# Optimization experiments

Hardware: AMD Instinct MI355X
Metric: run time of the kernel (lower is better)

## Reference

```python
import jax, jax.numpy as jnp
import numpy as np
import math

EPSILON = 1e-5
B, P, H, W = 64, 68, 64, 64


def setup_inputs() -> dict:
    key = jax.random.key(0)
    k1, k2, k3 = jax.random.split(key, 3)
    # probability heatmaps: positive, normalized over spatial dims
    hm = jax.random.uniform(k1, (B, P, H, W), dtype=jnp.float32) + 1e-3
    hm = hm / jnp.sum(hm, axis=(2, 3), keepdims=True)
    # means in pixel coordinates [0, W)
    means = jax.random.uniform(k2, (B, P, 2), dtype=jnp.float32) * (W - 1)
    # SPD 2x2 covariance, flattened to 4: Sigma = A A^T + c*I
    A = jax.random.normal(k3, (B, P, 2, 2), dtype=jnp.float32) * 2.0
    Sigma = jnp.einsum('bpij,bpkj->bpik', A, A) + 2.0 * jnp.eye(2, dtype=jnp.float32)
    covariance = Sigma.reshape(B, P, 4)
    return {"heatmaps": hm, "means": means, "covariance": covariance}


def reference(heatmaps, means, covariance):
    b, p, h, w = heatmaps.shape
    # grid: xv[i,j] = j, yv[i,j] = i
    yv, xv = jnp.meshgrid(jnp.arange(h, dtype=heatmaps.dtype),
                          jnp.arange(w, dtype=heatmaps.dtype), indexing='ij')
    Sigma = covariance.reshape(b, p, 2, 2)
    s00, s01 = Sigma[:, :, 0, 0], Sigma[:, :, 0, 1]
    s10, s11 = Sigma[:, :, 1, 0], Sigma[:, :, 1, 1]
    det = s00 * s11 - s01 * s10 + EPSILON                       # [b,p]
    # centered coordinates, [b,p,h,w]
    dx = xv[None, None] - means[:, :, 0, None, None]
    dy = yv[None, None] - means[:, :, 1, None, None]
    # quadratic form v^T Sigma^{-1} v with Sigma^{-1} = adj(Sigma)/det
    quad = (s11[..., None, None] * dx * dx
            - (s01 + s10)[..., None, None] * dx * dy
            + s00[..., None, None] * dy * dy) / det[..., None, None]
    log_prob_2 = -0.5 * quad
    prob = jnp.exp(log_prob_2) / (2.0 * math.pi * jnp.sqrt(det)[..., None, None])
    prob = prob / jnp.sum(prob, axis=(2, 3), keepdims=True)
    # KLDivLoss(reduce=False): target * (log target - input), target = heatmaps (detached)
    hm = heatmaps.reshape(b * p, h * w)
    pr = prob.reshape(b * p, h * w)
    kld = jax.scipy.special.xlogy(hm, hm) - hm * jnp.log(pr + EPSILON)
    loss = jnp.sum(kld, axis=1).mean()
    return loss
```

## Files before the change

kernel.cpp:

```cpp
#include <hip/hip_runtime.h>
#include <math.h>

#define EPS 1e-5f

constexpr int Bc = 64, Pc = 68, Hc = 64, Wc = 64;
constexpr int NPIX  = Hc * Wc;
constexpr int NTILE = Bc * Pc;
constexpr int BLK   = 256;
constexpr int PPT   = NPIX / BLK;

__device__ __forceinline__ float block_reduce_sum(float v, float* sbuf) {
    __syncthreads();
    #pragma unroll
    for (int o = 32; o > 0; o >>= 1) v += __shfl_down(v, o, 64);
    const int lane = threadIdx.x & 63;
    const int wid  = threadIdx.x >> 6;
    if (lane == 0) sbuf[wid] = v;
    __syncthreads();
    if (threadIdx.x == 0) {
        sbuf[4] = sbuf[0] + sbuf[1] + sbuf[2] + sbuf[3];
    }
    __syncthreads();
    return sbuf[4];
}

__global__ __launch_bounds__(BLK)
void gauss_kld_tile_kernel(const float* __restrict__ hm,
                           const float* __restrict__ means,
                           const float* __restrict__ cov,
                           float* __restrict__ partial) {
    const int tile = blockIdx.x;
    const float* __restrict__ h = hm + (size_t)tile * NPIX;
    const int t = threadIdx.x;

    const float4* __restrict__ h4p = reinterpret_cast<const float4*>(h);
    const float4 hv0 = h4p[0 * BLK + t];
    const float4 hv1 = h4p[1 * BLK + t];
    const float4 hv2 = h4p[2 * BLK + t];
    const float4 hv3 = h4p[3 * BLK + t];

    const float mx  = means[tile * 2 + 0];
    const float my  = means[tile * 2 + 1];
    const float s00 = cov[tile * 4 + 0];
    const float s01 = cov[tile * 4 + 1];
    const float s10 = cov[tile * 4 + 2];
    const float s11 = cov[tile * 4 + 3];
    const float det = s00 * s11 - s01 * s10 + EPS;
    const float inv_det = 1.0f / det;
    const float c_xx = -0.5f *  s11 * inv_det;
    const float c_xy =  0.5f * (s01 + s10) * inv_det;
    const float c_yy = -0.5f *  s00 * inv_det;

    auto lp_at = [&](int idx) -> float {
        const float dy = (float)(idx >> 6) - my;
        const float dx = (float)(idx & 63) - mx;
        return (c_xx * dx + c_xy * dy) * dx + c_yy * dy * dy;
    };

    float esum = 0.0f;
    #pragma unroll
    for (int k = 0; k < PPT / 4; k++) {
        const int base = (k * BLK + t) * 4;
        #pragma unroll
        for (int c = 0; c < 4; c++) {
            esum += __expf(lp_at(base + c));
        }
    }

    __shared__ float sbuf[8];
    const float S = block_reduce_sum(esum, sbuf);
    const float invS = 1.0f / S;

    auto kterm = [&](float hvi, int idx) -> float {
        const float pr = __expf(lp_at(idx)) * invS + EPS;
        return (hvi > 0.0f) ? hvi * __logf(__fdividef(hvi, pr)) : 0.0f;
    };

    float kl = 0.0f;
    #define PASS_B(h4v, kk)                            \
        {                                              \
            const int base = ((kk) * BLK + t) * 4;     \
            kl += kterm(h4v.x, base + 0);              \
            kl += kterm(h4v.y, base + 1);              \
            kl += kterm(h4v.z, base + 2);              \
            kl += kterm(h4v.w, base + 3);              \
        }
    PASS_B(hv0, 0)
    PASS_B(hv1, 1)
    PASS_B(hv2, 2)
    PASS_B(hv3, 3)
    #undef PASS_B

    const float tile_sum = block_reduce_sum(kl, sbuf);
    if (threadIdx.x == 0) partial[tile] = tile_sum;
}

__global__ __launch_bounds__(BLK)
void gauss_kld_reduce_kernel(const float* __restrict__ partial,
                             float* __restrict__ out) {
    float s = 0.0f;
    for (int i = threadIdx.x; i < NTILE; i += BLK) s += partial[i];
    __shared__ float sbuf[8];
    const float tot = block_reduce_sum(s, sbuf);
    if (threadIdx.x == 0) out[0] = tot / (float)NTILE;
}

extern "C" void kernel_launch(void* const* d_in, const int* in_sizes, int n_in,
                              void* d_out, int out_size, void* d_ws, size_t ws_size,
                              hipStream_t stream) {
    const float* hm    = (const float*)d_in[0];
    const float* means = (const float*)d_in[1];
    const float* cov   = (const float*)d_in[2];
    float* out = (float*)d_out;
    float* partial = (float*)d_ws;

    gauss_kld_tile_kernel<<<NTILE, BLK, 0, stream>>>(hm, means, cov, partial);
    gauss_kld_reduce_kernel<<<1, BLK, 0, stream>>>(partial, out);
}
```

Baseline: 112.4 us.

## Precompute Gaussian normalizers in separate kernel and fold log S algebraically

Moves the per-tile Gaussian normalizer sum into its own kernel, where each wave handles one tile with one lane per column, so each exp reuses separable x-terms. The KL kernel then skips the first exp pass and its block reduction. It rewrites log(p+eps) as log(e+eps*S) - log S, adding a second reduction of heatmap mass. The cost is one more kernel launch and a small global round-trip for S and log S.

```diff
diff --git a/kernel.cpp b/kernel.cpp
--- a/kernel.cpp
+++ b/kernel.cpp
@@ -3,9 +3,8 @@
 
 #define EPS 1e-5f
 
-constexpr int Bc = 64, Pc = 68, Hc = 64, Wc = 64;
-constexpr int NPIX  = Hc * Wc;
-constexpr int NTILE = Bc * Pc;
+constexpr int NPIX  = 4096;
+constexpr int NTILE = 4352;
 constexpr int BLK   = 256;
 constexpr int PPT   = NPIX / BLK;
 
@@ -17,18 +16,57 @@
     const int wid  = threadIdx.x >> 6;
     if (lane == 0) sbuf[wid] = v;
     __syncthreads();
-    if (threadIdx.x == 0) {
-        sbuf[4] = sbuf[0] + sbuf[1] + sbuf[2] + sbuf[3];
-    }
+    if (threadIdx.x == 0) sbuf[4] = sbuf[0] + sbuf[1] + sbuf[2] + sbuf[3];
     __syncthreads();
     return sbuf[4];
 }
 
 __global__ __launch_bounds__(BLK)
-void gauss_kld_tile_kernel(const float* __restrict__ hm,
-                           const float* __restrict__ means,
-                           const float* __restrict__ cov,
-                           float* __restrict__ partial) {
+void norm_kernel(const float* __restrict__ means,
+                 const float* __restrict__ cov,
+                 float* __restrict__ S_arr,
+                 float* __restrict__ logS_arr) {
+    const int lane = threadIdx.x & 63;
+    const int tile = blockIdx.x * 4 + (threadIdx.x >> 6);
+
+    const float mx  = means[tile * 2 + 0];
+    const float my  = means[tile * 2 + 1];
+    const float s00 = cov[tile * 4 + 0];
+    const float s01 = cov[tile * 4 + 1];
+    const float s10 = cov[tile * 4 + 2];
+    const float s11 = cov[tile * 4 + 3];
+    const float det = s00 * s11 - s01 * s10 + EPS;
+    const float inv_det = 1.0f / det;
+    const float cxx = -0.5f *  s11 * inv_det;
+    const float cxy =  0.5f * (s01 + s10) * inv_det;
+    const float cyy = -0.5f *  s00 * inv_det;
+
+    const float dx = (float)lane - mx;
+    const float qx = cxx * dx * dx;
+    const float bx = cxy * dx;
+
+    float s = 0.0f;
+    #pragma unroll
+    for (int y = 0; y < 64; y++) {
+        const float dy = (float)y - my;
+        const float lp = qx + (bx + cyy * dy) * dy;
+        s += __expf(lp);
+    }
+    #pragma unroll
+    for (int o = 32; o > 0; o >>= 1) s += __shfl_down(s, o, 64);
+    if (lane == 0) {
+        S_arr[tile]    = s;
+        logS_arr[tile] = __logf(s);
+    }
+}
+
+__global__ __launch_bounds__(BLK)
+void kl_kernel(const float* __restrict__ hm,
+               const float* __restrict__ means,
+               const float* __restrict__ cov,
+               const float* __restrict__ S_arr,
+               const float* __restrict__ logS_arr,
+               float* __restrict__ partial) {
     const int tile = blockIdx.x;
     const float* __restrict__ h = hm + (size_t)tile * NPIX;
     const int t = threadIdx.x;
@@ -47,57 +85,51 @@
     const float s11 = cov[tile * 4 + 3];
     const float det = s00 * s11 - s01 * s10 + EPS;
     const float inv_det = 1.0f / det;
-    const float c_xx = -0.5f *  s11 * inv_det;
-    const float c_xy =  0.5f * (s01 + s10) * inv_det;
-    const float c_yy = -0.5f *  s00 * inv_det;
+    const float cxx = -0.5f *  s11 * inv_det;
+    const float cxy =  0.5f * (s01 + s10) * inv_det;
+    const float cyy = -0.5f *  s00 * inv_det;
 
-    auto lp_at = [&](int idx) -> float {
+    const float S    = S_arr[tile];
+    const float logS = logS_arr[tile];
+    const float E    = EPS * S;
+
+    float kl = 0.0f;
+    float hs = 0.0f;
+
+    auto pixel = [&](float hv, int idx) {
         const float dy = (float)(idx >> 6) - my;
         const float dx = (float)(idx & 63) - mx;
-        return (c_xx * dx + c_xy * dy) * dx + c_yy * dy * dy;
+        const float lp = (cxx * dx + cxy * dy) * dx + cyy * dy * dy;
+        const float u  = __expf(lp) + E;
+        if (hv > 0.0f) {
+            kl += hv * __logf(__fdividef(hv, u));
+            hs += hv;
+        }
     };
 
-    float esum = 0.0f;
-    #pragma unroll
-    for (int k = 0; k < PPT / 4; k++) {
-        const int base = (k * BLK + t) * 4;
-        #pragma unroll
-        for (int c = 0; c < 4; c++) {
-            esum += __expf(lp_at(base + c));
+    #define GROUP(h4v, kk)                         \
+        {                                          \
+            const int base = ((kk) * BLK + t) * 4; \
+            pixel(h4v.x, base + 0);                \
+            pixel(h4v.y, base + 1);                \
+            pixel(h4v.z, base + 2);                \
+            pixel(h4v.w, base + 3);                \
         }
-    }
+    GROUP(hv0, 0)
+    GROUP(hv1, 1)
+    GROUP(hv2, 2)
+    GROUP(hv3, 3)
+    #undef GROUP
 
     __shared__ float sbuf[8];
-    const float S = block_reduce_sum(esum, sbuf);
-    const float invS = 1.0f / S;
-
-    auto kterm = [&](float hvi, int idx) -> float {
-        const float pr = __expf(lp_at(idx)) * invS + EPS;
-        return (hvi > 0.0f) ? hvi * __logf(__fdividef(hvi, pr)) : 0.0f;
-    };
-
-    float kl = 0.0f;
-    #define PASS_B(h4v, kk)                            \
-        {                                              \
-            const int base = ((kk) * BLK + t) * 4;     \
-            kl += kterm(h4v.x, base + 0);              \
-            kl += kterm(h4v.y, base + 1);              \
-            kl += kterm(h4v.z, base + 2);              \
-            kl += kterm(h4v.w, base + 3);              \
-        }
-    PASS_B(hv0, 0)
-    PASS_B(hv1, 1)
-    PASS_B(hv2, 2)
-    PASS_B(hv3, 3)
-    #undef PASS_B
-
-    const float tile_sum = block_reduce_sum(kl, sbuf);
-    if (threadIdx.x == 0) partial[tile] = tile_sum;
+    const float kl_sum = block_reduce_sum(kl, sbuf);
+    const float hs_sum = block_reduce_sum(hs, sbuf);
+    if (threadIdx.x == 0) partial[tile] = kl_sum + logS * hs_sum;
 }
 
 __global__ __launch_bounds__(BLK)
-void gauss_kld_reduce_kernel(const float* __restrict__ partial,
-                             float* __restrict__ out) {
+void reduce_kernel(const float* __restrict__ partial,
+                   float* __restrict__ out) {
     float s = 0.0f;
     for (int i = threadIdx.x; i < NTILE; i += BLK) s += partial[i];
     __shared__ float sbuf[8];
@@ -112,8 +144,12 @@
     const float* means = (const float*)d_in[1];
     const float* cov   = (const float*)d_in[2];
     float* out = (float*)d_out;
-    float* partial = (float*)d_ws;
 
-    gauss_kld_tile_kernel<<<NTILE, BLK, 0, stream>>>(hm, means, cov, partial);
-    gauss_kld_reduce_kernel<<<1, BLK, 0, stream>>>(partial, out);
+    float* S_arr    = (float*)d_ws;
+    float* logS_arr = S_arr + NTILE;
+    float* partial  = logS_arr + NTILE;
+
+    norm_kernel<<<NTILE / 4, BLK, 0, stream>>>(means, cov, S_arr, logS_arr);
+    kl_kernel<<<NTILE, BLK, 0, stream>>>(hm, means, cov, S_arr, logS_arr, partial);
+    reduce_kernel<<<1, BLK, 0, stream>>>(partial, out);
 }
```

Measured after the change: 116.0 us. 1.03x slower.
